# Optimization experiments

Hardware: AMD Instinct MI355X
Metric: run time of the kernel (lower is better)

Reference implementation:

```python
import jax, jax.numpy as jnp
import numpy as np

TANH_CONST = 2.5
TEMPERATURE = 5.0


def setup_inputs() -> dict:
    key = jax.random.key(0)
    ks = jax.random.split(key, 9)
    B, L, NB, H, NC = 16384, 64, 8, 128, 1000
    return {
        "class_ids": jax.random.randint(ks[0], (B,), 0, NC),
        "gumbel_u": jax.random.uniform(ks[1], (L, B, NB), dtype=jnp.float32),
        "g_emb": jax.random.normal(ks[2], (NC, H), dtype=jnp.float32) * 0.1,
        "w_emb": jax.random.normal(ks[3], (NB, H), dtype=jnp.float32) * 0.1,
        "w_soft": jax.random.normal(ks[4], (NB, H), dtype=jnp.float32) * 0.1,
        "w_ih": jax.random.normal(ks[5], (4 * H, H), dtype=jnp.float32) * 0.1,
        "w_hh": jax.random.normal(ks[6], (4 * H, H), dtype=jnp.float32) * 0.1,
        "b_ih": jax.random.normal(ks[7], (4 * H,), dtype=jnp.float32) * 0.1,
        "b_hh": jax.random.normal(ks[8], (4 * H,), dtype=jnp.float32) * 0.1,
    }


def reference(class_ids, gumbel_u, g_emb, w_emb, w_soft, w_ih, w_hh, b_ih, b_hh):
    B = class_ids.shape[0]
    H = g_emb.shape[1]
    x0 = g_emb[class_ids]                      # [B, H] class embedding (reused each step)
    h0 = jnp.zeros((B, H), x0.dtype)
    c0 = jnp.zeros((B, H), x0.dtype)

    def step(carry, u):
        h, c, x = carry
        gates = x @ w_ih.T + h @ w_hh.T + b_ih + b_hh   # [B, 4H], torch gate order i,f,g,o
        i, f, g, o = jnp.split(gates, 4, axis=-1)
        c2 = jax.nn.sigmoid(f) * c + jax.nn.sigmoid(i) * jnp.tanh(g)
        h2 = jax.nn.sigmoid(o) * jnp.tanh(c2)
        logit = h2 @ w_soft.T                           # [B, NB]
        logit = TANH_CONST * jnp.tanh(logit / TEMPERATURE)
        # categorical sample via gumbel-max
        uc = jnp.clip(u, 1e-8, 1.0 - 1e-8)
        gmb = -jnp.log(-jnp.log(uc))
        branch = jnp.argmax(logit + gmb, axis=-1)       # [B] int
        logp = jax.nn.log_softmax(logit, axis=-1)
        lp = jnp.take_along_axis(logp, branch[:, None], axis=1)[:, 0]
        ent = -jnp.sum(jnp.exp(logp) * logp, axis=-1)
        x2 = (w_emb[branch] + x0) * 0.5
        return (h2, c2, x2), (branch, lp, ent)

    _, (arcs, lps, ents) = jax.lax.scan(step, (h0, c0, x0), gumbel_u)
    # stack along dim=1 like torch.stack(..., dim=1) -> [B, L]
    sample_arc = arcs.T
    sample_log_prob = lps.T
    sample_entropy = ents.T
    sample_prob = jnp.exp(sample_log_prob)
    return sample_arc, sample_log_prob, sample_entropy, sample_prob
```

## Files before the change

kernel.cpp:

```cpp
#include <hip/hip_runtime.h>
#include <math.h>

#define HD 128
#define NBR 8
#define LSTEPS 64
#define TILE_B 64
#define HT_PAD 68
#define PART_PAD 65

#define WPT_OFF   0
#define WIPT_OFF  65536
#define PP_OFF    131072
#define BIH_OFF   135168
#define BHH_OFF   135680

__global__ __launch_bounds__(256) void setup_kernel(
    const float* __restrict__ w_emb, const float* __restrict__ w_ih,
    const float* __restrict__ w_hh, const float* __restrict__ b_ih,
    const float* __restrict__ b_hh, float* __restrict__ ws)
{
  int tid = blockIdx.x * blockDim.x + threadIdx.x;
  if (tid < 65536) {
    int k = tid >> 9, col = tid & 511;
    int hh = col >> 2, q = col & 3;
    ws[WPT_OFF + tid]  = w_hh[(q*HD + hh)*HD + k];
    ws[WIPT_OFF + tid] = w_ih[(q*HD + hh)*HD + k];
  }
  if (tid < 4096) {
    int j = tid >> 9, rem = tid & 511;
    int q = rem >> 7, hh2 = rem & 127;
    const float* wr = w_ih + (q*HD + hh2)*HD;
    const float* er = w_emb + j*HD;
    float s = 0.f;
    for (int k = 0; k < HD; ++k) s = fmaf(er[k], wr[k], s);
    ws[PP_OFF + (size_t)j*512 + q*HD + hh2] = s;
  }
  if (tid < 512) {
    int q = tid >> 7, hh2 = tid & 127;
    ws[BIH_OFF + tid] = b_ih[q*HD + hh2];
    ws[BHH_OFF + tid] = b_hh[q*HD + hh2];
  }
}

__global__ __launch_bounds__(512, 2) void ctrl_kernel(
    const int* __restrict__ class_ids,
    const float* __restrict__ gumbel_u,
    const float* __restrict__ g_emb,
    const float* __restrict__ w_soft,
    const float* __restrict__ ws,
    float* __restrict__ out,
    int Btot)
{
  __shared__ float hT[HD * HT_PAD];
  __shared__ float wsoft_l[NBR * HD];
  __shared__ float part_l[TILE_B * PART_PAD];
  __shared__ int   br_l[TILE_B];

  const int tid = threadIdx.x;
  const int b0  = blockIdx.x * TILE_B;
  const size_t BL = (size_t)Btot * LSTEPS;

  const float* __restrict__ wpT  = ws + WPT_OFF;
  const float* __restrict__ wipT = ws + WIPT_OFF;
  const float* __restrict__ Pp   = ws + PP_OFF;

  for (int i = tid; i < NBR*HD; i += 512) wsoft_l[i] = w_soft[i];

  const int hh = tid & 127;
  const int bg = tid >> 7;

  float bi[4], bh[4];
  #pragma unroll
  for (int q = 0; q < 4; ++q) {
    bi[q] = ws[BIH_OFF + q*HD + hh];
    bh[q] = ws[BHH_OFF + q*HD + hh];
  }

  {
    int sb = tid >> 3;
    int kc = tid & 7;
    int cid = class_ids[b0 + sb];
    const float* src = g_emb + (size_t)cid * HD + kc*16;
    #pragma unroll
    for (int ii = 0; ii < 4; ++ii) {
      float4 v = *(const float4*)(src + 4*ii);
      int kb = kc*16 + 4*ii;
      hT[(kb+0)*HT_PAD + sb] = v.x;
      hT[(kb+1)*HT_PAD + sb] = v.y;
      hT[(kb+2)*HT_PAD + sb] = v.z;
      hT[(kb+3)*HT_PAD + sb] = v.w;
    }
  }
  __syncthreads();

  float q0[4][16];
  #pragma unroll
  for (int q = 0; q < 4; ++q)
    #pragma unroll
    for (int j = 0; j < 16; ++j) q0[q][j] = 0.f;

  #pragma unroll 2
  for (int k = 0; k < HD; ++k) {
    float4 w = *(const float4*)(wipT + k*512 + 4*hh);
    const float* hr = &hT[k*HT_PAD + bg*16];
    float4 ha = *(const float4*)(hr);
    float4 hb2 = *(const float4*)(hr+4);
    float4 hc = *(const float4*)(hr+8);
    float4 hd = *(const float4*)(hr+12);
    float hv[16] = {ha.x,ha.y,ha.z,ha.w,hb2.x,hb2.y,hb2.z,hb2.w,
                    hc.x,hc.y,hc.z,hc.w,hd.x,hd.y,hd.z,hd.w};
    float wv[4] = {w.x,w.y,w.z,w.w};
    #pragma unroll
    for (int q = 0; q < 4; ++q)
      #pragma unroll
      for (int j = 0; j < 16; ++j)
        q0[q][j] = fmaf(hv[j], wv[q], q0[q][j]);
  }
  __syncthreads();

  float c[16];
  #pragma unroll
  for (int j = 0; j < 16; ++j) c[j] = 0.f;

  for (int t = 0; t < LSTEPS; ++t) {
    float4 ua = make_float4(0,0,0,0), ub = make_float4(0,0,0,0);
    if (tid < TILE_B) {
      const float* up = gumbel_u + ((size_t)t * Btot + (b0 + tid)) * NBR;
      ua = *(const float4*)up;
      ub = *(const float4*)(up + 4);
    }

    float acc[4][16];
    #pragma unroll
    for (int q = 0; q < 4; ++q)
      #pragma unroll
      for (int j = 0; j < 16; ++j) acc[q][j] = 0.f;

    if (t > 0) {
      #pragma unroll 2
      for (int k = 0; k < HD; ++k) {
        float4 w = *(const float4*)(wpT + k*512 + 4*hh);
        const float* hr = &hT[k*HT_PAD + bg*16];
        float4 ha = *(const float4*)(hr);
        float4 hb2 = *(const float4*)(hr+4);
        float4 hc = *(const float4*)(hr+8);
        float4 hd = *(const float4*)(hr+12);
        float hv[16] = {ha.x,ha.y,ha.z,ha.w,hb2.x,hb2.y,hb2.z,hb2.w,
                        hc.x,hc.y,hc.z,hc.w,hd.x,hd.y,hd.z,hd.w};
        float wv[4] = {w.x,w.y,w.z,w.w};
        #pragma unroll
        for (int q = 0; q < 4; ++q)
          #pragma unroll
          for (int j = 0; j < 16; ++j)
            acc[q][j] = fmaf(hv[j], wv[q], acc[q][j]);
      }
    }

    float h2v[16];
    #pragma unroll
    for (int j = 0; j < 16; ++j) {
      float xw[4];
      if (t == 0) {
        #pragma unroll
        for (int q = 0; q < 4; ++q) xw[q] = q0[q][j];
      } else {
        int br = br_l[bg*16 + j];
        const float* pr = Pp + (size_t)br*512 + hh;
        #pragma unroll
        for (int q = 0; q < 4; ++q) xw[q] = 0.5f * (pr[q*HD] + q0[q][j]);
      }
      float gi = ((xw[0] + acc[0][j]) + bi[0]) + bh[0];
      float gf = ((xw[1] + acc[1][j]) + bi[1]) + bh[1];
      float gg = ((xw[2] + acc[2][j]) + bi[2]) + bh[2];
      float go = ((xw[3] + acc[3][j]) + bi[3]) + bh[3];
      float iv = 1.f/(1.f + expf(-gi));
      float fv = 1.f/(1.f + expf(-gf));
      float gv = tanhf(gg);
      float ov = 1.f/(1.f + expf(-go));
      float c2 = fv*c[j] + iv*gv;
      c[j] = c2;
      h2v[j] = ov * tanhf(c2);
    }
    __syncthreads();

    {
      float* dst = &hT[hh*HT_PAD + bg*16];
      *(float4*)(dst)    = make_float4(h2v[0],h2v[1],h2v[2],h2v[3]);
      *(float4*)(dst+4)  = make_float4(h2v[4],h2v[5],h2v[6],h2v[7]);
      *(float4*)(dst+8)  = make_float4(h2v[8],h2v[9],h2v[10],h2v[11]);
      *(float4*)(dst+12) = make_float4(h2v[12],h2v[13],h2v[14],h2v[15]);
    }
    __syncthreads();

    {
      int lb = tid & 63, ch = tid >> 6;
      float part[8];
      #pragma unroll
      for (int nb = 0; nb < 8; ++nb) part[nb] = 0.f;
      #pragma unroll
      for (int i = 0; i < 16; ++i) {
        float hvv = hT[(ch*16 + i)*HT_PAD + lb];
        #pragma unroll
        for (int nb = 0; nb < 8; ++nb)
          part[nb] = fmaf(hvv, wsoft_l[nb*HD + ch*16 + i], part[nb]);
      }
      #pragma unroll
      for (int nb = 0; nb < 8; ++nb)
        part_l[lb*PART_PAD + nb*8 + ch] = part[nb];
    }
    __syncthreads();

    if (tid < TILE_B) {
      int lb = tid;
      float lg[8];
      #pragma unroll
      for (int nb = 0; nb < 8; ++nb) {
        float s = 0.f;
        #pragma unroll
        for (int ch = 0; ch < 8; ++ch) s += part_l[lb*PART_PAD + nb*8 + ch];
        lg[nb] = 2.5f * tanhf(s / 5.0f);
      }
      float uv[8] = {ua.x,ua.y,ua.z,ua.w,ub.x,ub.y,ub.z,ub.w};
      int br = 0; float best;
      {
        float uc = fminf(fmaxf(uv[0], 1e-8f), 0.99999999f);
        best = lg[0] - logf(-logf(uc));
      }
      #pragma unroll
      for (int nb = 1; nb < 8; ++nb) {
        float uc = fminf(fmaxf(uv[nb], 1e-8f), 0.99999999f);
        float y = lg[nb] - logf(-logf(uc));
        if (y > best) { best = y; br = nb; }
      }
      float m = lg[0];
      #pragma unroll
      for (int nb = 1; nb < 8; ++nb) m = fmaxf(m, lg[nb]);
      float se = 0.f;
      #pragma unroll
      for (int nb = 0; nb < 8; ++nb) se += expf(lg[nb] - m);
      float lse = logf(se);
      float lp = (lg[br] - m) - lse;
      float ent = 0.f;
      #pragma unroll
      for (int nb = 0; nb < 8; ++nb) {
        float lpi = (lg[nb] - m) - lse;
        ent -= expf(lpi) * lpi;
      }
      size_t row = (size_t)(b0 + lb) * LSTEPS + t;
      out[row]        = (float)br;
      out[BL + row]   = lp;
      out[2*BL + row] = ent;
      out[3*BL + row] = expf(lp);
      br_l[lb] = br;
    }
    __syncthreads();
  }
}

extern "C" void kernel_launch(void* const* d_in, const int* in_sizes, int n_in,
                              void* d_out, int out_size, void* d_ws, size_t ws_size,
                              hipStream_t stream) {
  const int*   class_ids = (const int*)d_in[0];
  const float* gumbel_u  = (const float*)d_in[1];
  const float* g_emb     = (const float*)d_in[2];
  const float* w_emb     = (const float*)d_in[3];
  const float* w_soft    = (const float*)d_in[4];
  const float* w_ih      = (const float*)d_in[5];
  const float* w_hh      = (const float*)d_in[6];
  const float* b_ih      = (const float*)d_in[7];
  const float* b_hh      = (const float*)d_in[8];
  float* out = (float*)d_out;
  float* ws  = (float*)d_ws;
  int B = in_sizes[0];

  hipLaunchKernelGGL(setup_kernel, dim3(256), dim3(256), 0, stream,
                     w_emb, w_ih, w_hh, b_ih, b_hh, ws);
  hipLaunchKernelGGL(ctrl_kernel, dim3(B / TILE_B), dim3(512), 0, stream,
                     class_ids, gumbel_u, g_emb, w_soft, ws, out, B);
}
```

Measured before the change: 2.176 ms.

## Halve batch tile, cache branch projections in LDS, parallelize sampling with shuffles

Halves the per-block batch tile to 32 and raises the occupancy target to 4 blocks per CU, cutting per-thread accumulators from 64 to 32 registers. The precomputed branch-embedding projections are prescaled by 0.5 and staged in shared memory instead of read from global, and the two biases are pre-summed. The softmax/gumbel sampling stage is redone so every thread handles one (row, branch) pair, using wave shuffles for the reductions instead of a 64-thread serial tail with an extra LDS round trip and barrier. It trades per-thread reuse of the weight loads (more blocks each re-read the recurrent weights) for more parallelism and latency hiding.

```diff
diff --git a/kernel.cpp b/kernel.cpp
--- a/kernel.cpp
+++ b/kernel.cpp
@@ -4,9 +4,9 @@
 #define HD 128
 #define NBR 8
 #define LSTEPS 64
-#define TILE_B 64
-#define HT_PAD 68
-#define PART_PAD 65
+#define TILE_B 32
+#define HT_PAD 36
+#define WS_PAD 132
 
 #define WPT_OFF   0
 #define WIPT_OFF  65536
@@ -33,7 +33,7 @@
     const float* er = w_emb + j*HD;
     float s = 0.f;
     for (int k = 0; k < HD; ++k) s = fmaf(er[k], wr[k], s);
-    ws[PP_OFF + (size_t)j*512 + q*HD + hh2] = s;
+    ws[PP_OFF + (size_t)j*512 + q*HD + hh2] = 0.5f * s;
   }
   if (tid < 512) {
     int q = tid >> 7, hh2 = tid & 127;
@@ -42,7 +42,7 @@
   }
 }
 
-__global__ __launch_bounds__(512, 2) void ctrl_kernel(
+__global__ __launch_bounds__(512, 4) void ctrl_kernel(
     const int* __restrict__ class_ids,
     const float* __restrict__ gumbel_u,
     const float* __restrict__ g_emb,
@@ -52,8 +52,8 @@
     int Btot)
 {
   __shared__ float hT[HD * HT_PAD];
-  __shared__ float wsoft_l[NBR * HD];
-  __shared__ float part_l[TILE_B * PART_PAD];
+  __shared__ float wsoft_l[NBR * WS_PAD];
+  __shared__ float pp_l[NBR * 512];
   __shared__ int   br_l[TILE_B];
 
   const int tid = threadIdx.x;
@@ -62,117 +62,120 @@
 
   const float* __restrict__ wpT  = ws + WPT_OFF;
   const float* __restrict__ wipT = ws + WIPT_OFF;
-  const float* __restrict__ Pp   = ws + PP_OFF;
-
-  for (int i = tid; i < NBR*HD; i += 512) wsoft_l[i] = w_soft[i];
+
+  for (int i = tid; i < NBR*HD; i += 512) {
+    int nb = i >> 7, k = i & 127;
+    wsoft_l[nb*WS_PAD + k] = w_soft[i];
+  }
+  for (int i = tid; i < NBR*512; i += 512) pp_l[i] = ws[PP_OFF + i];
 
   const int hh = tid & 127;
   const int bg = tid >> 7;
 
-  float bi[4], bh[4];
-  #pragma unroll
-  for (int q = 0; q < 4; ++q) {
-    bi[q] = ws[BIH_OFF + q*HD + hh];
-    bh[q] = ws[BHH_OFF + q*HD + hh];
-  }
-
-  {
-    int sb = tid >> 3;
-    int kc = tid & 7;
-    int cid = class_ids[b0 + sb];
-    const float* src = g_emb + (size_t)cid * HD + kc*16;
-    #pragma unroll
-    for (int ii = 0; ii < 4; ++ii) {
-      float4 v = *(const float4*)(src + 4*ii);
-      int kb = kc*16 + 4*ii;
-      hT[(kb+0)*HT_PAD + sb] = v.x;
-      hT[(kb+1)*HT_PAD + sb] = v.y;
-      hT[(kb+2)*HT_PAD + sb] = v.z;
-      hT[(kb+3)*HT_PAD + sb] = v.w;
-    }
-  }
-  __syncthreads();
-
-  float q0[4][16];
+  float bsum[4];
   #pragma unroll
   for (int q = 0; q < 4; ++q)
-    #pragma unroll
-    for (int j = 0; j < 16; ++j) q0[q][j] = 0.f;
-
-  #pragma unroll 2
+    bsum[q] = ws[BIH_OFF + q*HD + hh] + ws[BHH_OFF + q*HD + hh];
+
+  {
+    int sb = tid >> 4;
+    int kc = tid & 15;
+    int cid = class_ids[b0 + sb];
+    const float* src = g_emb + (size_t)cid * HD + kc*8;
+    float4 v0 = *(const float4*)(src);
+    float4 v1 = *(const float4*)(src + 4);
+    int kb = kc*8;
+    hT[(kb+0)*HT_PAD + sb] = v0.x;  hT[(kb+1)*HT_PAD + sb] = v0.y;
+    hT[(kb+2)*HT_PAD + sb] = v0.z;  hT[(kb+3)*HT_PAD + sb] = v0.w;
+    hT[(kb+4)*HT_PAD + sb] = v1.x;  hT[(kb+5)*HT_PAD + sb] = v1.y;
+    hT[(kb+6)*HT_PAD + sb] = v1.z;  hT[(kb+7)*HT_PAD + sb] = v1.w;
+  }
+  __syncthreads();
+
+  float q0[4][8];
+  #pragma unroll
+  for (int q = 0; q < 4; ++q)
+    #pragma unroll
+    for (int j = 0; j < 8; ++j) q0[q][j] = 0.f;
+
+  #pragma unroll 4
   for (int k = 0; k < HD; ++k) {
     float4 w = *(const float4*)(wipT + k*512 + 4*hh);
-    const float* hr = &hT[k*HT_PAD + bg*16];
+    const float* hr = &hT[k*HT_PAD + bg*8];
     float4 ha = *(const float4*)(hr);
-    float4 hb2 = *(const float4*)(hr+4);
-    float4 hc = *(const float4*)(hr+8);
-    float4 hd = *(const float4*)(hr+12);
-    float hv[16] = {ha.x,ha.y,ha.z,ha.w,hb2.x,hb2.y,hb2.z,hb2.w,
-                    hc.x,hc.y,hc.z,hc.w,hd.x,hd.y,hd.z,hd.w};
-    float wv[4] = {w.x,w.y,w.z,w.w};
+    float4 hb = *(const float4*)(hr+4);
+    #pragma unroll
+    for (int q = 0; q < 4; ++q) {
+      float wq = (q==0)?w.x:((q==1)?w.y:((q==2)?w.z:w.w));
+      q0[q][0] = fmaf(ha.x, wq, q0[q][0]);
+      q0[q][1] = fmaf(ha.y, wq, q0[q][1]);
+      q0[q][2] = fmaf(ha.z, wq, q0[q][2]);
+      q0[q][3] = fmaf(ha.w, wq, q0[q][3]);
+      q0[q][4] = fmaf(hb.x, wq, q0[q][4]);
+      q0[q][5] = fmaf(hb.y, wq, q0[q][5]);
+      q0[q][6] = fmaf(hb.z, wq, q0[q][6]);
+      q0[q][7] = fmaf(hb.w, wq, q0[q][7]);
+    }
+  }
+  __syncthreads();
+
+  float c[8];
+  #pragma unroll
+  for (int j = 0; j < 8; ++j) c[j] = 0.f;
+
+  const int s_nb = tid & 7;
+  const int s_kh = (tid >> 3) & 1;
+  const int s_lb = tid >> 4;
+  const int laneBase = (tid & 63) & ~7;
+
+  for (int t = 0; t < LSTEPS; ++t) {
+    float uv = gumbel_u[((size_t)t * Btot + (b0 + s_lb)) * NBR + s_nb];
+
+    float acc[4][8];
     #pragma unroll
     for (int q = 0; q < 4; ++q)
       #pragma unroll
-      for (int j = 0; j < 16; ++j)
-        q0[q][j] = fmaf(hv[j], wv[q], q0[q][j]);
-  }
-  __syncthreads();
-
-  float c[16];
-  #pragma unroll
-  for (int j = 0; j < 16; ++j) c[j] = 0.f;
-
-  for (int t = 0; t < LSTEPS; ++t) {
-    float4 ua = make_float4(0,0,0,0), ub = make_float4(0,0,0,0);
-    if (tid < TILE_B) {
-      const float* up = gumbel_u + ((size_t)t * Btot + (b0 + tid)) * NBR;
-      ua = *(const float4*)up;
-      ub = *(const float4*)(up + 4);
-    }
-
-    float acc[4][16];
-    #pragma unroll
-    for (int q = 0; q < 4; ++q)
-      #pragma unroll
-      for (int j = 0; j < 16; ++j) acc[q][j] = 0.f;
+      for (int j = 0; j < 8; ++j) acc[q][j] = 0.f;
 
     if (t > 0) {
-      #pragma unroll 2
+      #pragma unroll 4
       for (int k = 0; k < HD; ++k) {
         float4 w = *(const float4*)(wpT + k*512 + 4*hh);
-        const float* hr = &hT[k*HT_PAD + bg*16];
+        const float* hr = &hT[k*HT_PAD + bg*8];
         float4 ha = *(const float4*)(hr);
-        float4 hb2 = *(const float4*)(hr+4);
-        float4 hc = *(const float4*)(hr+8);
-        float4 hd = *(const float4*)(hr+12);
-        float hv[16] = {ha.x,ha.y,ha.z,ha.w,hb2.x,hb2.y,hb2.z,hb2.w,
-                        hc.x,hc.y,hc.z,hc.w,hd.x,hd.y,hd.z,hd.w};
-        float wv[4] = {w.x,w.y,w.z,w.w};
-        #pragma unroll
-        for (int q = 0; q < 4; ++q)
-          #pragma unroll
-          for (int j = 0; j < 16; ++j)
-            acc[q][j] = fmaf(hv[j], wv[q], acc[q][j]);
-      }
-    }
-
-    float h2v[16];
-    #pragma unroll
-    for (int j = 0; j < 16; ++j) {
+        float4 hb = *(const float4*)(hr+4);
+        #pragma unroll
+        for (int q = 0; q < 4; ++q) {
+          float wq = (q==0)?w.x:((q==1)?w.y:((q==2)?w.z:w.w));
+          acc[q][0] = fmaf(ha.x, wq, acc[q][0]);
+          acc[q][1] = fmaf(ha.y, wq, acc[q][1]);
+          acc[q][2] = fmaf(ha.z, wq, acc[q][2]);
+          acc[q][3] = fmaf(ha.w, wq, acc[q][3]);
+          acc[q][4] = fmaf(hb.x, wq, acc[q][4]);
+          acc[q][5] = fmaf(hb.y, wq, acc[q][5]);
+          acc[q][6] = fmaf(hb.z, wq, acc[q][6]);
+          acc[q][7] = fmaf(hb.w, wq, acc[q][7]);
+        }
+      }
+    }
+
+    float h2v[8];
+    #pragma unroll
+    for (int j = 0; j < 8; ++j) {
       float xw[4];
       if (t == 0) {
         #pragma unroll
         for (int q = 0; q < 4; ++q) xw[q] = q0[q][j];
       } else {
-        int br = br_l[bg*16 + j];
-        const float* pr = Pp + (size_t)br*512 + hh;
-        #pragma unroll
-        for (int q = 0; q < 4; ++q) xw[q] = 0.5f * (pr[q*HD] + q0[q][j]);
-      }
-      float gi = ((xw[0] + acc[0][j]) + bi[0]) + bh[0];
-      float gf = ((xw[1] + acc[1][j]) + bi[1]) + bh[1];
-      float gg = ((xw[2] + acc[2][j]) + bi[2]) + bh[2];
-      float go = ((xw[3] + acc[3][j]) + bi[3]) + bh[3];
+        int br = br_l[bg*8 + j];
+        const float* pr = &pp_l[br*512 + hh];
+        #pragma unroll
+        for (int q = 0; q < 4; ++q) xw[q] = pr[q*HD] + q0[q][j];
+      }
+      float gi = (xw[0] + acc[0][j]) + bsum[0];
+      float gf = (xw[1] + acc[1][j]) + bsum[1];
+      float gg = (xw[2] + acc[2][j]) + bsum[2];
+      float go = (xw[3] + acc[3][j]) + bsum[3];
       float iv = 1.f/(1.f + expf(-gi));
       float fv = 1.f/(1.f + expf(-gf));
       float gv = tanhf(gg);
@@ -181,77 +184,71 @@
       c[j] = c2;
       h2v[j] = ov * tanhf(c2);
     }
+    if (t == 0) {
+      #pragma unroll
+      for (int q = 0; q < 4; ++q)
+        #pragma unroll
+        for (int j = 0; j < 8; ++j) q0[q][j] *= 0.5f;
+    }
     __syncthreads();
 
     {
-      float* dst = &hT[hh*HT_PAD + bg*16];
-      *(float4*)(dst)    = make_float4(h2v[0],h2v[1],h2v[2],h2v[3]);
-      *(float4*)(dst+4)  = make_float4(h2v[4],h2v[5],h2v[6],h2v[7]);
-      *(float4*)(dst+8)  = make_float4(h2v[8],h2v[9],h2v[10],h2v[11]);
-      *(float4*)(dst+12) = make_float4(h2v[12],h2v[13],h2v[14],h2v[15]);
+      float* dst = &hT[hh*HT_PAD + bg*8];
+      *(float4*)(dst)   = make_float4(h2v[0],h2v[1],h2v[2],h2v[3]);
+      *(float4*)(dst+4) = make_float4(h2v[4],h2v[5],h2v[6],h2v[7]);
     }
     __syncthreads();
 
     {
-      int lb = tid & 63, ch = tid >> 6;
-      float part[8];
-      #pragma unroll
-      for (int nb = 0; nb < 8; ++nb) part[nb] = 0.f;
-      #pragma unroll
-      for (int i = 0; i < 16; ++i) {
-        float hvv = hT[(ch*16 + i)*HT_PAD + lb];
-        #pragma unroll
-        for (int nb = 0; nb < 8; ++nb)
-          part[nb] = fmaf(hvv, wsoft_l[nb*HD + ch*16 + i], part[nb]);
-      }
-      #pragma unroll
-      for (int nb = 0; nb < 8; ++nb)
-        part_l[lb*PART_PAD + nb*8 + ch] = part[nb];
-    }
-    __syncthreads();
-
-    if (tid < TILE_B) {
-      int lb = tid;
-      float lg[8];
-      #pragma unroll
-      for (int nb = 0; nb < 8; ++nb) {
-        float s = 0.f;
-        #pragma unroll
-        for (int ch = 0; ch < 8; ++ch) s += part_l[lb*PART_PAD + nb*8 + ch];
-        lg[nb] = 2.5f * tanhf(s / 5.0f);
-      }
-      float uv[8] = {ua.x,ua.y,ua.z,ua.w,ub.x,ub.y,ub.z,ub.w};
-      int br = 0; float best;
-      {
-        float uc = fminf(fmaxf(uv[0], 1e-8f), 0.99999999f);
-        best = lg[0] - logf(-logf(uc));
-      }
-      #pragma unroll
-      for (int nb = 1; nb < 8; ++nb) {
-        float uc = fminf(fmaxf(uv[nb], 1e-8f), 0.99999999f);
-        float y = lg[nb] - logf(-logf(uc));
-        if (y > best) { best = y; br = nb; }
-      }
-      float m = lg[0];
-      #pragma unroll
-      for (int nb = 1; nb < 8; ++nb) m = fmaxf(m, lg[nb]);
-      float se = 0.f;
-      #pragma unroll
-      for (int nb = 0; nb < 8; ++nb) se += expf(lg[nb] - m);
+      float s = 0.f;
+      const int kb = s_kh * 64;
+      #pragma unroll 8
+      for (int i = 0; i < 64; ++i) {
+        int k = kb + i;
+        s = fmaf(hT[k*HT_PAD + s_lb], wsoft_l[s_nb*WS_PAD + k], s);
+      }
+      s += __shfl_xor(s, 8);
+      float lg = 2.5f * tanhf(s * 0.2f);
+
+      float uc  = fminf(fmaxf(uv, 1e-8f), 0.99999999f);
+      float y   = lg - logf(-logf(uc));
+      int   idx = s_nb;
+      #pragma unroll
+      for (int mask = 1; mask <= 4; mask <<= 1) {
+        float oy  = __shfl_xor(y, mask);
+        int   oi  = __shfl_xor(idx, mask);
+        if (oy > y || (oy == y && oi < idx)) { y = oy; idx = oi; }
+      }
+      float m = lg;
+      #pragma unroll
+      for (int mask = 1; mask <= 4; mask <<= 1)
+        m = fmaxf(m, __shfl_xor(m, mask));
+      float e = expf(lg - m);
+      float se = e;
+      #pragma unroll
+      for (int mask = 1; mask <= 4; mask <<= 1)
+        se += __shfl_xor(se, mask);
       float lse = logf(se);
-      float lp = (lg[br] - m) - lse;
-      float ent = 0.f;
-      #pragma unroll
-      for (int nb = 0; nb < 8; ++nb) {
-        float lpi = (lg[nb] - m) - lse;
-        ent -= expf(lpi) * lpi;
-      }
-      size_t row = (size_t)(b0 + lb) * LSTEPS + t;
-      out[row]        = (float)br;
-      out[BL + row]   = lp;
-      out[2*BL + row] = ent;
-      out[3*BL + row] = expf(lp);
-      br_l[lb] = br;
+      float lpi = (lg - m) - lse;
+      float pi  = e / se;
+      float epi = pi * lpi;
+      float ent = epi;
+      #pragma unroll
+      for (int mask = 1; mask <= 4; mask <<= 1)
+        ent += __shfl_xor(ent, mask);
+      ent = -ent;
+      int srcLane = laneBase | idx;
+      float lp_sel = __shfl(lpi, srcLane);
+      float pr_sel = __shfl(pi,  srcLane);
+
+      if ((tid & 15) == 0) {
+        size_t row = (size_t)(b0 + s_lb) * LSTEPS + t;
+        out[row]        = (float)idx;
+        out[BL + row]   = lp_sel;
+        out[2*BL + row] = ent;
+        out[3*BL + row] = pr_sel;
+        br_l[s_lb] = idx;
+      }
     }
     __syncthreads();
   }
```

Result: slower. 2.320 ms (+6.6%).

## Halve batch tile, relayout gate weights per-thread, cache P in LDS, use fast math

Applied to the files above, without the earlier changes.

Cuts the per-block batch tile to 32 rows with 256 threads, so twice as many blocks are launched. Gate weights are re-laid out so each thread streams its own contiguous k-row. The emb·W_ih projections are prescaled by 0.5 and kept in LDS, and the two bias vectors are pre-summed and folded into the class-embedding term after step 0. Sigmoid, tanh, log and exp now use fast rcp/exp intrinsics to cut transcendental cost in the recurrent loop. The risks are lower accuracy from the approximate math, and weight reads that are strided across lanes and now rely on cache rather than coalescing.

```diff
diff --git a/kernel.cpp b/kernel.cpp
--- a/kernel.cpp
+++ b/kernel.cpp
@@ -4,15 +4,21 @@
 #define HD 128
 #define NBR 8
 #define LSTEPS 64
-#define TILE_B 64
-#define HT_PAD 68
+#define TILE_B 32
+#define HT_PAD 36
 #define PART_PAD 65
 
-#define WPT_OFF   0
-#define WIPT_OFF  65536
+#define WHH2_OFF  0
+#define WIH2_OFF  65536
 #define PP_OFF    131072
-#define BIH_OFF   135168
-#define BHH_OFF   135680
+#define BS_OFF    135168
+
+__device__ __forceinline__ float fsig(float x) {
+  return __builtin_amdgcn_rcpf(1.f + __expf(-x));
+}
+__device__ __forceinline__ float ftanh(float x) {
+  return 1.f - 2.f * __builtin_amdgcn_rcpf(1.f + __expf(2.f * x));
+}
 
 __global__ __launch_bounds__(256) void setup_kernel(
     const float* __restrict__ w_emb, const float* __restrict__ w_ih,
@@ -21,28 +27,23 @@
 {
   int tid = blockIdx.x * blockDim.x + threadIdx.x;
   if (tid < 65536) {
-    int k = tid >> 9, col = tid & 511;
-    int hh = col >> 2, q = col & 3;
-    ws[WPT_OFF + tid]  = w_hh[(q*HD + hh)*HD + k];
-    ws[WIPT_OFF + tid] = w_ih[(q*HD + hh)*HD + k];
+    int hh = tid >> 9, k = (tid >> 2) & 127, q = tid & 3;
+    ws[WHH2_OFF + tid] = w_hh[(q*HD + hh)*HD + k];
+    ws[WIH2_OFF + tid] = w_ih[(q*HD + hh)*HD + k];
   }
   if (tid < 4096) {
     int j = tid >> 9, rem = tid & 511;
-    int q = rem >> 7, hh2 = rem & 127;
+    int hh2 = rem >> 2, q = rem & 3;
     const float* wr = w_ih + (q*HD + hh2)*HD;
     const float* er = w_emb + j*HD;
     float s = 0.f;
     for (int k = 0; k < HD; ++k) s = fmaf(er[k], wr[k], s);
-    ws[PP_OFF + (size_t)j*512 + q*HD + hh2] = s;
-  }
-  if (tid < 512) {
-    int q = tid >> 7, hh2 = tid & 127;
-    ws[BIH_OFF + tid] = b_ih[q*HD + hh2];
-    ws[BHH_OFF + tid] = b_hh[q*HD + hh2];
-  }
-}
-
-__global__ __launch_bounds__(512, 2) void ctrl_kernel(
+    ws[PP_OFF + tid] = 0.5f * s;
+  }
+  if (tid < 512) ws[BS_OFF + tid] = b_ih[tid] + b_hh[tid];
+}
+
+__global__ __launch_bounds__(256, 2) void ctrl_kernel(
     const int* __restrict__ class_ids,
     const float* __restrict__ gumbel_u,
     const float* __restrict__ g_emb,
@@ -52,7 +53,8 @@
     int Btot)
 {
   __shared__ float hT[HD * HT_PAD];
-  __shared__ float wsoft_l[NBR * HD];
+  __shared__ float ws_l[NBR * HD];
+  __shared__ float pp_l[NBR * HD * 4];
   __shared__ float part_l[TILE_B * PART_PAD];
   __shared__ int   br_l[TILE_B];
 
@@ -60,21 +62,19 @@
   const int b0  = blockIdx.x * TILE_B;
   const size_t BL = (size_t)Btot * LSTEPS;
 
-  const float* __restrict__ wpT  = ws + WPT_OFF;
-  const float* __restrict__ wipT = ws + WIPT_OFF;
-  const float* __restrict__ Pp   = ws + PP_OFF;
-
-  for (int i = tid; i < NBR*HD; i += 512) wsoft_l[i] = w_soft[i];
+  for (int i = tid; i < NBR*HD; i += 256) ws_l[i] = w_soft[i];
+  for (int i = tid; i < NBR*HD*4; i += 256) pp_l[i] = ws[PP_OFF + i];
 
   const int hh = tid & 127;
   const int bg = tid >> 7;
 
-  float bi[4], bh[4];
+  float bsq[4];
   #pragma unroll
-  for (int q = 0; q < 4; ++q) {
-    bi[q] = ws[BIH_OFF + q*HD + hh];
-    bh[q] = ws[BHH_OFF + q*HD + hh];
-  }
+  for (int q = 0; q < 4; ++q) bsq[q] = ws[BS_OFF + q*HD + hh];
+
+  const float* __restrict__ whhp = ws + WHH2_OFF + hh*512;
+  const float* __restrict__ wihp = ws + WIH2_OFF + hh*512;
+  const float* hTb = hT + bg*16;
 
   {
     int sb = tid >> 3;
@@ -99,22 +99,26 @@
     #pragma unroll
     for (int j = 0; j < 16; ++j) q0[q][j] = 0.f;
 
-  #pragma unroll 2
+  #pragma unroll 8
   for (int k = 0; k < HD; ++k) {
-    float4 w = *(const float4*)(wipT + k*512 + 4*hh);
-    const float* hr = &hT[k*HT_PAD + bg*16];
-    float4 ha = *(const float4*)(hr);
-    float4 hb2 = *(const float4*)(hr+4);
-    float4 hc = *(const float4*)(hr+8);
-    float4 hd = *(const float4*)(hr+12);
-    float hv[16] = {ha.x,ha.y,ha.z,ha.w,hb2.x,hb2.y,hb2.z,hb2.w,
-                    hc.x,hc.y,hc.z,hc.w,hd.x,hd.y,hd.z,hd.w};
-    float wv[4] = {w.x,w.y,w.z,w.w};
+    float4 w = *(const float4*)(wihp + k*4);
+    const float* hr = hTb + k*HT_PAD;
+    float4 h0 = *(const float4*)(hr);
+    float4 h1 = *(const float4*)(hr+4);
+    float4 h2 = *(const float4*)(hr+8);
+    float4 h3 = *(const float4*)(hr+12);
     #pragma unroll
-    for (int q = 0; q < 4; ++q)
-      #pragma unroll
-      for (int j = 0; j < 16; ++j)
-        q0[q][j] = fmaf(hv[j], wv[q], q0[q][j]);
+    for (int q = 0; q < 4; ++q) {
+      float wq = (q==0)?w.x:((q==1)?w.y:((q==2)?w.z:w.w));
+      q0[q][0]=fmaf(h0.x,wq,q0[q][0]); q0[q][1]=fmaf(h0.y,wq,q0[q][1]);
+      q0[q][2]=fmaf(h0.z,wq,q0[q][2]); q0[q][3]=fmaf(h0.w,wq,q0[q][3]);
+      q0[q][4]=fmaf(h1.x,wq,q0[q][4]); q0[q][5]=fmaf(h1.y,wq,q0[q][5]);
+      q0[q][6]=fmaf(h1.z,wq,q0[q][6]); q0[q][7]=fmaf(h1.w,wq,q0[q][7]);
+      q0[q][8]=fmaf(h2.x,wq,q0[q][8]); q0[q][9]=fmaf(h2.y,wq,q0[q][9]);
+      q0[q][10]=fmaf(h2.z,wq,q0[q][10]); q0[q][11]=fmaf(h2.w,wq,q0[q][11]);
+      q0[q][12]=fmaf(h3.x,wq,q0[q][12]); q0[q][13]=fmaf(h3.y,wq,q0[q][13]);
+      q0[q][14]=fmaf(h3.z,wq,q0[q][14]); q0[q][15]=fmaf(h3.w,wq,q0[q][15]);
+    }
   }
   __syncthreads();
 
@@ -130,56 +134,64 @@
       ub = *(const float4*)(up + 4);
     }
 
-    float acc[4][16];
-    #pragma unroll
-    for (int q = 0; q < 4; ++q)
-      #pragma unroll
-      for (int j = 0; j < 16; ++j) acc[q][j] = 0.f;
-
-    if (t > 0) {
-      #pragma unroll 2
+    float h2v[16];
+
+    if (t == 0) {
+      #pragma unroll
+      for (int j = 0; j < 16; ++j) {
+        float gi = q0[0][j] + bsq[0];
+        float gf = q0[1][j] + bsq[1];
+        float gg = q0[2][j] + bsq[2];
+        float go = q0[3][j] + bsq[3];
+        float c2 = fsig(gf)*c[j] + fsig(gi)*ftanh(gg);
+        c[j] = c2;
+        h2v[j] = fsig(go) * ftanh(c2);
+      }
+      #pragma unroll
+      for (int q = 0; q < 4; ++q)
+        #pragma unroll
+        for (int j = 0; j < 16; ++j) q0[q][j] = fmaf(q0[q][j], 0.5f, bsq[q]);
+    } else {
+      float acc[4][16];
+      #pragma unroll
+      for (int q = 0; q < 4; ++q)
+        #pragma unroll
+        for (int j = 0; j < 16; ++j) acc[q][j] = 0.f;
+
+      #pragma unroll 8
       for (int k = 0; k < HD; ++k) {
-        float4 w = *(const float4*)(wpT + k*512 + 4*hh);
-        const float* hr = &hT[k*HT_PAD + bg*16];
-        float4 ha = *(const float4*)(hr);
-        float4 hb2 = *(const float4*)(hr+4);
-        float4 hc = *(const float4*)(hr+8);
-        float4 hd = *(const float4*)(hr+12);
-        float hv[16] = {ha.x,ha.y,ha.z,ha.w,hb2.x,hb2.y,hb2.z,hb2.w,
-                        hc.x,hc.y,hc.z,hc.w,hd.x,hd.y,hd.z,hd.w};
-        float wv[4] = {w.x,w.y,w.z,w.w};
-        #pragma unroll
-        for (int q = 0; q < 4; ++q)
-          #pragma unroll
-          for (int j = 0; j < 16; ++j)
-            acc[q][j] = fmaf(hv[j], wv[q], acc[q][j]);
-      }
-    }
-
-    float h2v[16];
-    #pragma unroll
-    for (int j = 0; j < 16; ++j) {
-      float xw[4];
-      if (t == 0) {
-        #pragma unroll
-        for (int q = 0; q < 4; ++q) xw[q] = q0[q][j];
-      } else {
+        float4 w = *(const float4*)(whhp + k*4);
+        const float* hr = hTb + k*HT_PAD;
+        float4 h0 = *(const float4*)(hr);
+        float4 h1 = *(const float4*)(hr+4);
+        float4 h2 = *(const float4*)(hr+8);
+        float4 h3 = *(const float4*)(hr+12);
+        #pragma unroll
+        for (int q = 0; q < 4; ++q) {
+          float wq = (q==0)?w.x:((q==1)?w.y:((q==2)?w.z:w.w));
+          acc[q][0]=fmaf(h0.x,wq,acc[q][0]); acc[q][1]=fmaf(h0.y,wq,acc[q][1]);
+          acc[q][2]=fmaf(h0.z,wq,acc[q][2]); acc[q][3]=fmaf(h0.w,wq,acc[q][3]);
+          acc[q][4]=fmaf(h1.x,wq,acc[q][4]); acc[q][5]=fmaf(h1.y,wq,acc[q][5]);
+          acc[q][6]=fmaf(h1.z,wq,acc[q][6]); acc[q][7]=fmaf(h1.w,wq,acc[q][7]);
+          acc[q][8]=fmaf(h2.x,wq,acc[q][8]); acc[q][9]=fmaf(h2.y,wq,acc[q][9]);
+          acc[q][10]=fmaf(h2.z,wq,acc[q][10]); acc[q][11]=fmaf(h2.w,wq,acc[q][11]);
+          acc[q][12]=fmaf(h3.x,wq,acc[q][12]); acc[q][13]=fmaf(h3.y,wq,acc[q][13]);
+          acc[q][14]=fmaf(h3.z,wq,acc[q][14]); acc[q][15]=fmaf(h3.w,wq,acc[q][15]);
+        }
+      }
+
+      #pragma unroll
+      for (int j = 0; j < 16; ++j) {
         int br = br_l[bg*16 + j];
-        const float* pr = Pp + (size_t)br*512 + hh;
-        #pragma unroll
-        for (int q = 0; q < 4; ++q) xw[q] = 0.5f * (pr[q*HD] + q0[q][j]);
-      }
-      float gi = ((xw[0] + acc[0][j]) + bi[0]) + bh[0];
-      float gf = ((xw[1] + acc[1][j]) + bi[1]) + bh[1];
-      float gg = ((xw[2] + acc[2][j]) + bi[2]) + bh[2];
-      float go = ((xw[3] + acc[3][j]) + bi[3]) + bh[3];
-      float iv = 1.f/(1.f + expf(-gi));
-      float fv = 1.f/(1.f + expf(-gf));
-      float gv = tanhf(gg);
-      float ov = 1.f/(1.f + expf(-go));
-      float c2 = fv*c[j] + iv*gv;
-      c[j] = c2;
-      h2v[j] = ov * tanhf(c2);
+        float4 pv = *(const float4*)(&pp_l[(br*HD + hh)*4]);
+        float gi = (acc[0][j] + q0[0][j]) + pv.x;
+        float gf = (acc[1][j] + q0[1][j]) + pv.y;
+        float gg = (acc[2][j] + q0[2][j]) + pv.z;
+        float go = (acc[3][j] + q0[3][j]) + pv.w;
+        float c2 = fsig(gf)*c[j] + fsig(gi)*ftanh(gg);
+        c[j] = c2;
+        h2v[j] = fsig(go) * ftanh(c2);
+      }
     }
     __syncthreads();
 
@@ -193,7 +205,7 @@
     __syncthreads();
 
     {
-      int lb = tid & 63, ch = tid >> 6;
+      int lb = tid & 31, ch = tid >> 5;
       float part[8];
       #pragma unroll
       for (int nb = 0; nb < 8; ++nb) part[nb] = 0.f;
@@ -202,7 +214,7 @@
         float hvv = hT[(ch*16 + i)*HT_PAD + lb];
         #pragma unroll
         for (int nb = 0; nb < 8; ++nb)
-          part[nb] = fmaf(hvv, wsoft_l[nb*HD + ch*16 + i], part[nb]);
+          part[nb] = fmaf(hvv, ws_l[nb*HD + ch*16 + i], part[nb]);
       }
       #pragma unroll
       for (int nb = 0; nb < 8; ++nb)
@@ -218,18 +230,18 @@
         float s = 0.f;
         #pragma unroll
         for (int ch = 0; ch < 8; ++ch) s += part_l[lb*PART_PAD + nb*8 + ch];
-        lg[nb] = 2.5f * tanhf(s / 5.0f);
+        lg[nb] = 2.5f * ftanh(s * 0.2f);
       }
       float uv[8] = {ua.x,ua.y,ua.z,ua.w,ub.x,ub.y,ub.z,ub.w};
       int br = 0; float best;
       {
         float uc = fminf(fmaxf(uv[0], 1e-8f), 0.99999999f);
-        best = lg[0] - logf(-logf(uc));
+        best = lg[0] - __logf(-__logf(uc));
       }
       #pragma unroll
       for (int nb = 1; nb < 8; ++nb) {
         float uc = fminf(fmaxf(uv[nb], 1e-8f), 0.99999999f);
-        float y = lg[nb] - logf(-logf(uc));
+        float y = lg[nb] - __logf(-__logf(uc));
         if (y > best) { best = y; br = nb; }
       }
       float m = lg[0];
@@ -237,20 +249,20 @@
       for (int nb = 1; nb < 8; ++nb) m = fmaxf(m, lg[nb]);
       float se = 0.f;
       #pragma unroll
-      for (int nb = 0; nb < 8; ++nb) se += expf(lg[nb] - m);
-      float lse = logf(se);
+      for (int nb = 0; nb < 8; ++nb) se += __expf(lg[nb] - m);
+      float lse = __logf(se);
       float lp = (lg[br] - m) - lse;
       float ent = 0.f;
       #pragma unroll
       for (int nb = 0; nb < 8; ++nb) {
         float lpi = (lg[nb] - m) - lse;
-        ent -= expf(lpi) * lpi;
+        ent -= __expf(lpi) * lpi;
       }
       size_t row = (size_t)(b0 + lb) * LSTEPS + t;
       out[row]        = (float)br;
       out[BL + row]   = lp;
       out[2*BL + row] = ent;
-      out[3*BL + row] = expf(lp);
+      out[3*BL + row] = __expf(lp);
       br_l[lb] = br;
     }
     __syncthreads();
@@ -275,6 +287,6 @@
 
   hipLaunchKernelGGL(setup_kernel, dim3(256), dim3(256), 0, stream,
                      w_emb, w_ih, w_hh, b_ih, b_hh, ws);
-  hipLaunchKernelGGL(ctrl_kernel, dim3(B / TILE_B), dim3(512), 0, stream,
+  hipLaunchKernelGGL(ctrl_kernel, dim3(B / TILE_B), dim3(256), 0, stream,
                      class_ids, gumbel_u, g_emb, w_soft, ws, out, B);
 }
```

Result: slower. 2.225 ms (+2.3%).
